# Optimization experiments

Hardware: AMD Instinct MI355X
Metric: run time of the kernel (lower is better)

Reference implementation:

```python
import jax, jax.numpy as jnp
import numpy as np

S = 4096          # seq_len (longformer-large-4096)
H = 1024          # hidden_size
FF = 3072         # ffnn_size (hardcoded)
G = 100           # number of gold mentions
MAX_SPAN = 30     # max_span_length
TOP_LAMBDA = 0.2
LN_EPS = 1e-5
MASK_VAL = 10000.0


def setup_inputs() -> dict:
    key = jax.random.key(0)
    ks = jax.random.split(key, 16)
    sc = 0.02
    sequence_output = jax.random.normal(ks[0], (1, S, H), jnp.float32)
    attention_mask = jnp.ones((1, S), jnp.int32)
    # valid gold spans: 1 <= start <= end < start + MAX_SPAN (so torch's >0 filter keeps all)
    gs = jax.random.randint(ks[1], (G,), 1, S - MAX_SPAN)
    gl = jax.random.randint(ks[2], (G,), 0, MAX_SPAN)
    gold_mentions = jnp.stack([gs, gs + gl], axis=1).astype(jnp.int32)  # [G, 2]
    inp = {
        'sequence_output': sequence_output,
        'attention_mask': attention_mask,
        'gold_mentions': gold_mentions,
        # start_mention_mlp
        'W_sm': jax.random.normal(ks[3], (H, FF), jnp.float32) * sc,
        'b_sm': jnp.zeros((FF,), jnp.float32),
        'g_sm': jnp.ones((FF,), jnp.float32),
        'beta_sm': jnp.zeros((FF,), jnp.float32),
        # end_mention_mlp
        'W_em': jax.random.normal(ks[4], (H, FF), jnp.float32) * sc,
        'b_em': jnp.zeros((FF,), jnp.float32),
        'g_em': jnp.ones((FF,), jnp.float32),
        'beta_em': jnp.zeros((FF,), jnp.float32),
        # classifiers
        'w_start': jax.random.normal(ks[5], (FF,), jnp.float32) * sc,
        'b_start': jnp.zeros((), jnp.float32),
        'w_end': jax.random.normal(ks[6], (FF,), jnp.float32) * sc,
        'b_end': jnp.zeros((), jnp.float32),
        'W_s2e': jax.random.normal(ks[7], (FF, FF), jnp.float32) * sc,
        'b_s2e': jnp.zeros((FF,), jnp.float32),
    }
    return inp


def _fcl(x, W, b, g, beta):
    # dense -> gelu (exact) -> layernorm (dropout is identity in eval)
    h = jax.nn.gelu(x @ W + b, approximate=False)
    mu = jnp.mean(h, axis=-1, keepdims=True)
    var = jnp.mean(jnp.square(h - mu), axis=-1, keepdims=True)
    return (h - mu) * jax.lax.rsqrt(var + LN_EPS) * g + beta


def _forward(sequence_output, attention_mask, gold_mentions,
             W_sm, b_sm, g_sm, beta_sm, W_em, b_em, g_em, beta_em,
             w_start, b_start, w_end, b_end, W_s2e, b_s2e):
    start_reps = _fcl(sequence_output, W_sm, b_sm, g_sm, beta_sm)  # [1,S,FF]
    end_reps = _fcl(sequence_output, W_em, b_em, g_em, beta_em)    # [1,S,FF]

    start_logits = jnp.einsum('bsf,f->bs', start_reps, w_start) + b_start  # [1,S]
    end_logits = jnp.einsum('bsf,f->bs', end_reps, w_end) + b_end          # [1,S]
    temp = start_reps @ W_s2e + b_s2e                                      # [1,S,FF]
    joint = jnp.einsum('bsf,btf->bst', temp, end_reps)                     # [1,S,S]
    mention_logits = joint + start_logits[:, :, None] + end_logits[:, None, :]

    # span mask: start <= end < start + MAX_SPAN (triu(0) then tril(MAX_SPAN-1))
    i = jnp.arange(S)
    mention_mask = ((i[:, None] <= i[None, :]) & (i[None, :] < i[:, None] + MAX_SPAN)
                    ).astype(jnp.float32)[None]  # [1,S,S]
    mention_logits = jnp.clip(mention_logits + (1.0 - mention_mask) * (-MASK_VAL),
                              -MASK_VAL, MASK_VAL)

    # top-k pruning; attention_mask is full so k is static: int(S * 0.2)
    max_k = int(S * TOP_LAMBDA)  # 819
    _, topk_1d = jax.lax.top_k(mention_logits.reshape(1, -1), max_k)  # [1,max_k]
    sorted_idx = jnp.sort(topk_1d, axis=-1)
    topk_start_ids = sorted_idx // S
    topk_end_ids = sorted_idx % S
    span_mask = jnp.ones((1, max_k), jnp.float32)

    # losses
    probs = jax.nn.sigmoid(mention_logits)  # [1,S,S]
    gstart = gold_mentions[:, 0]
    gend = gold_mentions[:, 1]
    gold_probs = probs[0, gstart, gend]
    # torch BCE clamps log at -100
    cost_gold = -jnp.mean(jnp.maximum(jnp.log(gold_probs), -100.0))
    junk = probs.at[0, gstart, gend].set(0.0)
    log1mp = jnp.maximum(jnp.log(1.0 - junk), -100.0)
    cost_junk = -jnp.sum(jnp.where(mention_mask == 1.0, log1mp, 0.0)) / jnp.sum(mention_mask)
    cost_is_mention = (cost_gold + cost_junk)[None]  # [1]

    return topk_start_ids, topk_end_ids, span_mask, sequence_output, cost_is_mention


def reference(sequence_output, attention_mask, gold_mentions,
              W_sm, b_sm, g_sm, beta_sm, W_em, b_em, g_em, beta_em,
              w_start, b_start, w_end, b_end, W_s2e, b_s2e):
    return _forward(sequence_output, attention_mask, gold_mentions,
                    W_sm, b_sm, g_sm, beta_sm, W_em, b_em, g_em, beta_em,
                    w_start, b_start, w_end, b_end, W_s2e, b_s2e)
```

## Files before the change

### kernel.cpp

```cpp
#include <hip/hip_runtime.h>
#include <math.h>

#define S 4096
#define H 1024
#define FF 3072
#define G 100
#define MAXSPAN 30
#define MAXK 819
#define NBAND (S * MAXSPAN)
#define BAND_COUNT 122445.0

#define O_START 0
#define O_END   819
#define O_MASK  1638
#define O_SEQ   2457
#define O_COST  (2457 + S * H)

typedef __bf16 bf16x8 __attribute__((ext_vector_type(8)));
typedef float f32x16 __attribute__((ext_vector_type(16)));


__device__ __forceinline__ float block_reduce_256(float x, volatile float* red) {
  #pragma unroll
  for (int off = 32; off > 0; off >>= 1) x += __shfl_down(x, off, 64);
  int wid = threadIdx.x >> 6;
  int lane = threadIdx.x & 63;
  __syncthreads();
  if (lane == 0) red[wid] = x;
  __syncthreads();
  return red[0] + red[1] + red[2] + red[3];
}

__device__ __forceinline__ float block_reduce_1024(float x, volatile float* red) {
  #pragma unroll
  for (int off = 32; off > 0; off >>= 1) x += __shfl_down(x, off, 64);
  int wid = threadIdx.x >> 6;
  int lane = threadIdx.x & 63;
  __syncthreads();
  if (lane == 0) red[wid] = x;
  __syncthreads();
  float s = 0.f;
  #pragma unroll
  for (int q = 0; q < 16; q++) s += red[q];
  return s;
}

__device__ __forceinline__ unsigned f2key(float f) {
  unsigned b = __float_as_uint(f);
  return (b & 0x80000000u) ? ~b : (b | 0x80000000u);
}

__device__ __forceinline__ unsigned short bf16_rne(float x) {
  unsigned u = __float_as_uint(x);
  unsigned r = ((u >> 16) & 1u) + 0x7FFFu;
  return (unsigned short)((u + r) >> 16);
}

__device__ __forceinline__ void split2(float x, unsigned short& h, unsigned short& l) {
  h = bf16_rne(x);
  float hf = __uint_as_float(((unsigned)h) << 16);
  l = bf16_rne(x - hf);
}

__device__ __forceinline__ void gld16(const void* g, void* l) {
  __builtin_amdgcn_global_load_lds(
      (const __attribute__((address_space(1))) unsigned int*)g,
      (__attribute__((address_space(3))) unsigned int*)l, 16, 0, 0);
}


__device__ __forceinline__ void pack_a_body(const float* __restrict__ A,
                                            float* __restrict__ Aout,
                                            unsigned short* __restrict__ hi,
                                            unsigned short* __restrict__ lo,
                                            int K, int bx, int by) {
  __shared__ float tile[32][33];
  const int t = threadIdx.x;
  const int tx = t & 31, ty8 = t >> 5;
  const int k0 = bx * 32, r0 = by * 32;
  #pragma unroll
  for (int r = ty8; r < 32; r += 8) {
    float v = A[(size_t)(r0 + r) * K + k0 + tx];
    tile[r][tx] = v;
    if (Aout) Aout[(size_t)(r0 + r) * K + k0 + tx] = v;
  }
  __syncthreads();
  if (t < 128) {
    const int kql = t >> 5;
    const int rl = t & 31;
    unsigned short h8[8], l8[8];
    #pragma unroll
    for (int s = 0; s < 8; s++) split2(tile[rl][kql * 8 + s], h8[s], l8[s]);
    const size_t panel = (size_t)(r0 >> 7);
    const int rloc = (r0 & 127) + rl;
    const size_t off = panel * (size_t)(128 * K) + (size_t)(k0 / 8 + kql) * 1024 + (size_t)rloc * 8;
    *(uint4*)(hi + off) = *(const uint4*)h8;
    *(uint4*)(lo + off) = *(const uint4*)l8;
  }
}

__device__ __forceinline__ void pack_ln_a_body(const float* __restrict__ A,
                                               const float* __restrict__ mu,
                                               const float* __restrict__ rstd,
                                               const float* __restrict__ g,
                                               const float* __restrict__ beta,
                                               unsigned short* __restrict__ hi,
                                               unsigned short* __restrict__ lo,
                                               int K, int bx, int by) {
  __shared__ float tile[32][33];
  const int t = threadIdx.x;
  const int tx = t & 31, ty8 = t >> 5;
  const int k0 = bx * 32, r0 = by * 32;
  #pragma unroll
  for (int r = ty8; r < 32; r += 8)
    tile[r][tx] = A[(size_t)(r0 + r) * K + k0 + tx];
  __syncthreads();
  if (t < 128) {
    const int kql = t >> 5;
    const int rl = t & 31;
    const int row = r0 + rl;
    const float m = mu[row], rs = rstd[row];
    float4 g0 = *(const float4*)(g + k0 + kql * 8);
    float4 g1 = *(const float4*)(g + k0 + kql * 8 + 4);
    float4 b0 = *(const float4*)(beta + k0 + kql * 8);
    float4 b1 = *(const float4*)(beta + k0 + kql * 8 + 4);
    float gv[8] = {g0.x, g0.y, g0.z, g0.w, g1.x, g1.y, g1.z, g1.w};
    float bv[8] = {b0.x, b0.y, b0.z, b0.w, b1.x, b1.y, b1.z, b1.w};
    unsigned short h8[8], l8[8];
    #pragma unroll
    for (int s = 0; s < 8; s++) {
      float v = (tile[rl][kql * 8 + s] - m) * rs * gv[s] + bv[s];
      split2(v, h8[s], l8[s]);
    }
    const size_t panel = (size_t)(r0 >> 7);
    const int rloc = (r0 & 127) + rl;
    const size_t off = panel * (size_t)(128 * K) + (size_t)(k0 / 8 + kql) * 1024 + (size_t)rloc * 8;
    *(uint4*)(hi + off) = *(const uint4*)h8;
    *(uint4*)(lo + off) = *(const uint4*)l8;
  }
}

__device__ __forceinline__ void pack_bt_body(const float* __restrict__ W,
                                             unsigned short* __restrict__ hi,
                                             unsigned short* __restrict__ lo,
                                             int K, int N, int bx, int by) {
  __shared__ float tile[32][33];
  const int t = threadIdx.x;
  const int tx = t & 31, ty8 = t >> 5;
  const int k0 = bx * 32, n0 = by * 32;
  #pragma unroll
  for (int r = ty8; r < 32; r += 8)
    tile[r][tx] = W[(size_t)(k0 + r) * N + n0 + tx];
  __syncthreads();
  if (t < 128) {
    const int kql = t >> 5;
    const int nl = t & 31;
    unsigned short h8[8], l8[8];
    #pragma unroll
    for (int s = 0; s < 8; s++) split2(tile[kql * 8 + s][nl], h8[s], l8[s]);
    const size_t panel = (size_t)(n0 >> 7);
    const int nloc = (n0 & 127) + nl;
    const size_t off = panel * (size_t)(128 * K) + (size_t)(k0 / 8 + kql) * 1024 + (size_t)nloc * 8;
    *(uint4*)(hi + off) = *(const uint4*)h8;
    *(uint4*)(lo + off) = *(const uint4*)l8;
  }
}

__global__ __launch_bounds__(256) void pack_head_kernel(const float* __restrict__ seq,
                                                        float* __restrict__ seq_out,
                                                        unsigned short* __restrict__ sh,
                                                        unsigned short* __restrict__ sl,
                                                        const float* __restrict__ W1,
                                                        const float* __restrict__ W2,
                                                        unsigned short* __restrict__ w1h,
                                                        unsigned short* __restrict__ w1l,
                                                        unsigned short* __restrict__ w2h,
                                                        unsigned short* __restrict__ w2l) {
  const int y = blockIdx.y;
  if (y < 128)      pack_a_body(seq, seq_out, sh, sl, H, blockIdx.x, y);
  else if (y < 224) pack_bt_body(W1, w1h, w1l, H, FF, blockIdx.x, y - 128);
  else              pack_bt_body(W2, w2h, w2l, H, FF, blockIdx.x, y - 224);
}

__global__ __launch_bounds__(256) void pack_mid_kernel(const float* __restrict__ bufS,
                                                       const float* __restrict__ muS,
                                                       const float* __restrict__ rstdS,
                                                       const float* __restrict__ g,
                                                       const float* __restrict__ beta,
                                                       unsigned short* __restrict__ ahi,
                                                       unsigned short* __restrict__ alo,
                                                       const float* __restrict__ Ws2e,
                                                       unsigned short* __restrict__ wbh,
                                                       unsigned short* __restrict__ wbl) {
  const int y = blockIdx.y;
  if (y < 128) pack_ln_a_body(bufS, muS, rstdS, g, beta, ahi, alo, FF, blockIdx.x, y);
  else         pack_bt_body(Ws2e, wbh, wbl, FF, FF, blockIdx.x, y - 128);
}


template <int EPI>
__device__ __forceinline__ void gemm_body(const char* cAh, const char* cAl,
                                          const char* cBh, const char* cBl,
                                          const float* __restrict__ bias,
                                          float* __restrict__ C,
                                          int bm, int bn, int N, int K,
                                          char* smem) {
  const int tid = threadIdx.x;
  const int lane = tid & 63;
  const int wid = __builtin_amdgcn_readfirstlane(tid >> 6);
  const int wm = wid >> 1, wn = wid & 1;
  const int lb = lane * 16;
  const int ldsq = wid * 2048;

  const int khalf = lane >> 5;
  const int r31 = lane & 31;
  const int abase = khalf * 2048 + (wm * 64 + r31) * 16;
  const int bbase = khalf * 2048 + (wn * 64 + r31) * 16;

  f32x16 acc[2][2];
  #pragma unroll
  for (int a = 0; a < 2; a++)
    #pragma unroll
    for (int b = 0; b < 2; b++)
      #pragma unroll
      for (int r = 0; r < 16; r++) acc[a][b][r] = 0.0f;

  auto stage = [&](int buf, int k0) {
    const size_t qb = (size_t)((k0 >> 3) + wid) * 2048 + lb;
    char* sbuf = smem + buf * 32768 + ldsq;
    gld16(cAh + qb,        sbuf +     0);
    gld16(cAh + qb + 1024, sbuf +     0 + 1024);
    gld16(cAl + qb,        sbuf +  8192);
    gld16(cAl + qb + 1024, sbuf +  8192 + 1024);
    gld16(cBh + qb,        sbuf + 16384);
    gld16(cBh + qb + 1024, sbuf + 16384 + 1024);
    gld16(cBl + qb,        sbuf + 24576);
    gld16(cBl + qb + 1024, sbuf + 24576 + 1024);
  };

  stage(0, 0);
  for (int k0 = 0; k0 < K; k0 += 32) {
    const int cur = (k0 >> 5) & 1;
    __syncthreads();
    if (k0 + 32 < K) stage(cur ^ 1, k0 + 32);
    const char* sm = smem + cur * 32768;

    bf16x8 ah[2][2], al[2][2], bh[2][2], bl[2][2];
    #pragma unroll
    for (int ks = 0; ks < 2; ks++) {
      #pragma unroll
      for (int mt = 0; mt < 2; mt++) {
        ah[ks][mt] = *(const bf16x8*)(sm +     0 + ks * 4096 + abase + mt * 512);
        al[ks][mt] = *(const bf16x8*)(sm +  8192 + ks * 4096 + abase + mt * 512);
      }
      #pragma unroll
      for (int nt = 0; nt < 2; nt++) {
        bh[ks][nt] = *(const bf16x8*)(sm + 16384 + ks * 4096 + bbase + nt * 512);
        bl[ks][nt] = *(const bf16x8*)(sm + 24576 + ks * 4096 + bbase + nt * 512);
      }
    }
    #pragma unroll
    for (int ks = 0; ks < 2; ks++)
      #pragma unroll
      for (int mt = 0; mt < 2; mt++)
        #pragma unroll
        for (int nt = 0; nt < 2; nt++) {
          acc[mt][nt] = __builtin_amdgcn_mfma_f32_32x32x16_bf16(ah[ks][mt], bh[ks][nt], acc[mt][nt], 0, 0, 0);
          acc[mt][nt] = __builtin_amdgcn_mfma_f32_32x32x16_bf16(al[ks][mt], bh[ks][nt], acc[mt][nt], 0, 0, 0);
          acc[mt][nt] = __builtin_amdgcn_mfma_f32_32x32x16_bf16(ah[ks][mt], bl[ks][nt], acc[mt][nt], 0, 0, 0);
        }
  }

  #pragma unroll
  for (int mt = 0; mt < 2; mt++) {
    #pragma unroll
    for (int nt = 0; nt < 2; nt++) {
      const int colg = bn + wn * 64 + nt * 32 + r31;
      const float bb = bias[colg];
      #pragma unroll
      for (int reg = 0; reg < 16; reg++) {
        const int rowl = (reg & 3) + 8 * (reg >> 2) + 4 * khalf;
        const int rowg = bm + wm * 64 + mt * 32 + rowl;
        float v = acc[mt][nt][reg] + bb;
        if (EPI == 1) v = 0.5f * v * (1.0f + erff(v * 0.70710678118654752f));
        C[(size_t)rowg * N + colg] = v;
      }
    }
  }
}

__global__ __launch_bounds__(256) void gemm_mfma_kernel(const unsigned short* __restrict__ Ahi,
                                                        const unsigned short* __restrict__ Alo,
                                                        const unsigned short* __restrict__ Bhi,
                                                        const unsigned short* __restrict__ Blo,
                                                        const float* __restrict__ bias,
                                                        float* __restrict__ C,
                                                        int N, int K) {
  __shared__ __align__(16) char smem[65536];
  const size_t panAb = (size_t)blockIdx.y * (size_t)(128 * K) * 2;
  const size_t panBb = (size_t)blockIdx.x * (size_t)(128 * K) * 2;
  gemm_body<0>((const char*)Ahi + panAb, (const char*)Alo + panAb,
               (const char*)Bhi + panBb, (const char*)Blo + panBb,
               bias, C, blockIdx.y * 128, blockIdx.x * 128, N, K, smem);
}

__global__ __launch_bounds__(256) void gemm_mfma_dual_kernel(const unsigned short* __restrict__ Ahi,
                                                             const unsigned short* __restrict__ Alo,
                                                             const unsigned short* __restrict__ B1hi,
                                                             const unsigned short* __restrict__ B1lo,
                                                             const unsigned short* __restrict__ B2hi,
                                                             const unsigned short* __restrict__ B2lo,
                                                             const float* __restrict__ bias1,
                                                             const float* __restrict__ bias2,
                                                             float* __restrict__ C1,
                                                             float* __restrict__ C2,
                                                             int N, int K) {
  __shared__ __align__(16) char smem[65536];
  const int zb = blockIdx.z;
  const unsigned short* Bhi = zb ? B2hi : B1hi;
  const unsigned short* Blo = zb ? B2lo : B1lo;
  const float* bias = zb ? bias2 : bias1;
  float* C = zb ? C2 : C1;
  const size_t panAb = (size_t)blockIdx.y * (size_t)(128 * K) * 2;
  const size_t panBb = (size_t)blockIdx.x * (size_t)(128 * K) * 2;
  gemm_body<1>((const char*)Ahi + panAb, (const char*)Alo + panAb,
               (const char*)Bhi + panBb, (const char*)Blo + panBb,
               bias, C, blockIdx.y * 128, blockIdx.x * 128, N, K, smem);
}


__global__ __launch_bounds__(256) void ln_stats_kernel(const float* __restrict__ HbS,
                                                       const float* __restrict__ HbE,
                                                       const float* __restrict__ gS,
                                                       const float* __restrict__ betaS,
                                                       const float* __restrict__ wS,
                                                       const float* __restrict__ bS,
                                                       const float* __restrict__ gE,
                                                       const float* __restrict__ betaE,
                                                       const float* __restrict__ wE,
                                                       const float* __restrict__ bE,
                                                       float* __restrict__ slog,
                                                       float* __restrict__ elog,
                                                       float* __restrict__ muS,
                                                       float* __restrict__ rstdS,
                                                       float* __restrict__ muE,
                                                       float* __restrict__ rstdE) {
  __shared__ float red[4];
  const int row = blockIdx.x, tid = threadIdx.x;
  const int br = blockIdx.y;
  const float* Hb = br ? HbE : HbS;
  const float* g = br ? gE : gS;
  const float* beta = br ? betaE : betaS;
  const float* w = br ? wE : wS;
  const float* bsc = br ? bE : bS;
  const float* h = Hb + (size_t)row * FF;

  float4 v[3];
  float s = 0.0f;
  #pragma unroll
  for (int t = 0; t < 3; t++) {
    v[t] = *(const float4*)(h + tid * 4 + t * 1024);
    s += v[t].x + v[t].y + v[t].z + v[t].w;
  }
  float mu = block_reduce_256(s, red) * (1.0f / (float)FF);

  float s2 = 0.0f;
  #pragma unroll
  for (int t = 0; t < 3; t++) {
    float dx = v[t].x - mu, dy = v[t].y - mu, dz = v[t].z - mu, dw = v[t].w - mu;
    s2 += dx * dx + dy * dy + dz * dz + dw * dw;
  }
  float var = block_reduce_256(s2, red) * (1.0f / (float)FF);
  float rstd = rsqrtf(var + 1e-5f);

  float dot = 0.0f;
  #pragma unroll
  for (int t = 0; t < 3; t++) {
    int idx = tid * 4 + t * 1024;
    float4 gv = *(const float4*)(g + idx);
    float4 bv = *(const float4*)(beta + idx);
    float4 wv = *(const float4*)(w + idx);
    float rx = (v[t].x - mu) * rstd * gv.x + bv.x;
    float ry = (v[t].y - mu) * rstd * gv.y + bv.y;
    float rz = (v[t].z - mu) * rstd * gv.z + bv.z;
    float rw = (v[t].w - mu) * rstd * gv.w + bv.w;
    dot += rx * wv.x + ry * wv.y + rz * wv.z + rw * wv.w;
  }
  float dt = block_reduce_256(dot, red);
  if (tid == 0) {
    if (br) { elog[row] = dt + bsc[0]; muE[row] = mu; rstdE[row] = rstd; }
    else    { slog[row] = dt + bsc[0]; muS[row] = mu; rstdS[row] = rstd; }
  }
}


__global__ __launch_bounds__(256) void band_joint_kernel(const float* __restrict__ T,
                                                         const float* __restrict__ Eraw,
                                                         const float* __restrict__ muE,
                                                         const float* __restrict__ rstdE,
                                                         const float* __restrict__ gE,
                                                         const float* __restrict__ betaE,
                                                         const float* __restrict__ sl,
                                                         const float* __restrict__ el,
                                                         float* __restrict__ band,
                                                         double* __restrict__ jacc,
                                                         unsigned* __restrict__ hist16) {
  __shared__ float Elds[45][260];
  __shared__ float red[4];
  const int t = threadIdx.x;
  const int bx = blockIdx.x;
  const int sbx = (bx & 7) * 32 + (bx >> 3);
  const int i0 = sbx * 16;
  const int r_l = t >> 4, c = t & 15;

  float accd[MAXSPAN];
  #pragma unroll
  for (int d = 0; d < MAXSPAN; d++) accd[d] = 0.0f;

  for (int k0 = 0; k0 < FF; k0 += 256) {
    const float* trow = T + (size_t)(i0 + r_l) * FF + k0 + c * 16;
    float4 tv0 = *(const float4*)(trow + 0);
    float4 tv1 = *(const float4*)(trow + 4);
    float4 tv2 = *(const float4*)(trow + 8);
    float4 tv3 = *(const float4*)(trow + 12);
    __syncthreads();
    for (int rr = t >> 6; rr < 45; rr += 4) {
      int gr = i0 + rr;
      int cc = (t & 63) * 4;
      float4 rv = {0.f, 0.f, 0.f, 0.f};
      if (gr < S) {
        float4 ev = *(const float4*)(Eraw + (size_t)gr * FF + k0 + cc);
        float m = muE[gr], rs = rstdE[gr];
        float4 gv = *(const float4*)(gE + k0 + cc);
        float4 bv = *(const float4*)(betaE + k0 + cc);
        rv.x = (ev.x - m) * rs * gv.x + bv.x;
        rv.y = (ev.y - m) * rs * gv.y + bv.y;
        rv.z = (ev.z - m) * rs * gv.z + bv.z;
        rv.w = (ev.w - m) * rs * gv.w + bv.w;
      }
      *(float4*)&Elds[rr][cc] = rv;
    }
    __syncthreads();
    #pragma unroll
    for (int d = 0; d < MAXSPAN; d++) {
      const float* er = &Elds[r_l + d][c * 16];
      float4 e0 = *(const float4*)(er + 0);
      float4 e1 = *(const float4*)(er + 4);
      float4 e2 = *(const float4*)(er + 8);
      float4 e3 = *(const float4*)(er + 12);
      accd[d] += tv0.x * e0.x + tv0.y * e0.y + tv0.z * e0.z + tv0.w * e0.w
               + tv1.x * e1.x + tv1.y * e1.y + tv1.z * e1.z + tv1.w * e1.w
               + tv2.x * e2.x + tv2.y * e2.y + tv2.z * e2.z + tv2.w * e2.w
               + tv3.x * e3.x + tv3.y * e3.y + tv3.z * e3.z + tv3.w * e3.w;
    }
  }

  const int i = i0 + r_l;
  const float my_sl = sl[i];
  float jsum = 0.0f;
  #pragma unroll
  for (int d = 0; d < MAXSPAN; d++) {
    float v = accd[d];
    v += __shfl_down(v, 8, 16);
    v += __shfl_down(v, 4, 16);
    v += __shfl_down(v, 2, 16);
    v += __shfl_down(v, 1, 16);
    if (c == 0) {
      int j = i + d;
      if (j < S) {
        float vv = v + my_sl + el[j];
        vv = fminf(fmaxf(vv, -10000.0f), 10000.0f);
        band[i * MAXSPAN + d] = vv;
        atomicAdd(&hist16[f2key(vv) >> 16], 1u);
        float p = 1.0f / (1.0f + expf(-vv));
        jsum += fmaxf(logf(1.0f - p), -100.0f);
      } else {
        band[i * MAXSPAN + d] = -1e30f;
      }
    }
  }
  float tot = block_reduce_256(jsum, red);
  if (t == 0) atomicAdd(jacc, (double)tot);
}


__global__ __launch_bounds__(1024) void topk_finalize_kernel(const float* __restrict__ band,
                                                             const int* __restrict__ gold,
                                                             const double* __restrict__ jacc,
                                                             const unsigned* __restrict__ hist16,
                                                             float* __restrict__ out) {
  __shared__ int csum[1024];
  __shared__ unsigned sh_T16;
  __shared__ int sh_remk;
  __shared__ int sh_chunk, sh_above;
  __shared__ int idxbuf[1024];
  __shared__ unsigned tkey[256];
  __shared__ int tidx[256];
  __shared__ int cnt_gt, cnt_eq;
  __shared__ int sb[1024];
  __shared__ int gcell[G];
  __shared__ float redf[16];
  const int tid = threadIdx.x;

  int s = 0;
  #pragma unroll 8
  for (int q = 0; q < 64; q++) s += (int)hist16[tid * 64 + q];
  csum[tid] = s;
  __syncthreads();
  for (int off = 1; off < 1024; off <<= 1) {
    int v = (tid + off < 1024) ? csum[tid + off] : 0;
    __syncthreads();
    csum[tid] += v;
    __syncthreads();
  }
  {
    int nxt = (tid < 1023) ? csum[tid + 1] : 0;
    if (csum[tid] >= MAXK && nxt < MAXK) { sh_chunk = tid; sh_above = nxt; }
  }
  __syncthreads();
  if (tid == 0) {
    int cum = sh_above;
    int b = sh_chunk * 64 + 63;
    for (;; b--) {
      int h = (int)hist16[b];
      if (cum + h >= MAXK || b == sh_chunk * 64) { sh_T16 = (unsigned)b; sh_remk = MAXK - cum; break; }
      cum += h;
    }
  }
  __syncthreads();
  const unsigned T16 = sh_T16;
  int remk = sh_remk;

  if (tid == 0) { cnt_gt = 0; cnt_eq = 0; }
  __syncthreads();
  for (int e = tid; e < NBAND; e += 1024) {
    unsigned key = f2key(band[e]);
    unsigned k16 = key >> 16;
    if (k16 >= T16) {
      int i = e / MAXSPAN, d = e - i * MAXSPAN;
      int fi = i * S + i + d;
      if (k16 > T16) {
        int p = atomicAdd(&cnt_gt, 1);
        if (p < 1024) idxbuf[p] = fi;
      } else {
        int p = atomicAdd(&cnt_eq, 1);
        if (p < 256) { tkey[p] = key; tidx[p] = fi; }
      }
    }
  }
  __syncthreads();
  if (tid == 0) {
    int ngt = cnt_gt < 1024 ? cnt_gt : 1024;
    int ne = cnt_eq < 256 ? cnt_eq : 256;
    for (int a2 = 1; a2 < ne; a2++) {
      unsigned kv = tkey[a2]; int iv = tidx[a2];
      int b2 = a2 - 1;
      while (b2 >= 0 && (tkey[b2] < kv || (tkey[b2] == kv && tidx[b2] > iv))) {
        tkey[b2 + 1] = tkey[b2]; tidx[b2 + 1] = tidx[b2]; b2--;
      }
      tkey[b2 + 1] = kv; tidx[b2 + 1] = iv;
    }
    int take = remk < ne ? remk : ne;
    for (int q = 0; q < take; q++)
      if (ngt + q < 1024) idxbuf[ngt + q] = tidx[q];
  }
  __syncthreads();

  sb[tid] = (tid < MAXK) ? idxbuf[tid] : 0x7FFFFFFF;
  __syncthreads();
  for (int ksz = 2; ksz <= 1024; ksz <<= 1) {
    for (int jj = ksz >> 1; jj > 0; jj >>= 1) {
      int ixj = tid ^ jj;
      if (ixj > tid) {
        int a2 = sb[tid], b2 = sb[ixj];
        bool up = ((tid & ksz) == 0);
        if (up ? (a2 > b2) : (a2 < b2)) { sb[tid] = b2; sb[ixj] = a2; }
      }
      __syncthreads();
    }
  }
  if (tid < MAXK) {
    int fi = sb[tid];
    out[O_START + tid] = (float)(fi >> 12);
    out[O_END + tid]   = (float)(fi & 4095);
    out[O_MASK + tid]  = 1.0f;
  }

  if (tid < G) {
    int gs = gold[2 * tid], ge = gold[2 * tid + 1];
    gcell[tid] = gs * MAXSPAN + (ge - gs);
  }
  __syncthreads();
  float tg = 0.0f, tj = 0.0f;
  if (tid < G) {
    int cell = gcell[tid];
    float x = band[cell];
    float p = 1.0f / (1.0f + expf(-x));
    tg = fmaxf(logf(p), -100.0f);
    bool first = true;
    for (int q = 0; q < tid; q++)
      if (gcell[q] == cell) { first = false; break; }
    if (first) tj = fmaxf(logf(1.0f - p), -100.0f);
  }
  float sg = block_reduce_1024(tg, redf);
  float sj = block_reduce_1024(tj, redf);
  if (tid == 0) {
    double junk = *jacc - (double)sj;
    double cost = -((double)sg / (double)G) - (junk / BAND_COUNT);
    out[O_COST] = (float)cost;
  }
}


extern "C" void kernel_launch(void* const* d_in, const int* in_sizes, int n_in,
                              void* d_out, int out_size, void* d_ws, size_t ws_size,
                              hipStream_t stream) {
  (void)in_sizes; (void)n_in; (void)out_size; (void)ws_size;
  const float* seq    = (const float*)d_in[0];
  const int*   gold   = (const int*)d_in[2];
  const float* W_sm   = (const float*)d_in[3];
  const float* b_sm   = (const float*)d_in[4];
  const float* g_sm   = (const float*)d_in[5];
  const float* be_sm  = (const float*)d_in[6];
  const float* W_em   = (const float*)d_in[7];
  const float* b_em   = (const float*)d_in[8];
  const float* g_em   = (const float*)d_in[9];
  const float* be_em  = (const float*)d_in[10];
  const float* w_st   = (const float*)d_in[11];
  const float* b_st   = (const float*)d_in[12];
  const float* w_en   = (const float*)d_in[13];
  const float* b_en   = (const float*)d_in[14];
  const float* W_s2e  = (const float*)d_in[15];
  const float* b_s2e  = (const float*)d_in[16];
  float* out = (float*)d_out;
  char* ws = (char*)d_ws;

  const size_t SZ_REP = (size_t)S * FF * 4;
  float*  bufS = (float*)(ws);
  float*  bufE = (float*)(ws + SZ_REP);
  float*  bufT = (float*)(ws + 2 * SZ_REP);
  char* R3 = ws + 3 * SZ_REP;
  unsigned short* seqhi = (unsigned short*)R3;
  unsigned short* seqlo = (unsigned short*)(R3 + (size_t)S * H * 2);
  unsigned short* a3hi  = (unsigned short*)R3;
  unsigned short* a3lo  = (unsigned short*)(R3 + (size_t)S * FF * 2);
  char* R4 = ws + 4 * SZ_REP;
  const size_t SZ_W12 = (size_t)H * FF * 2;
  unsigned short* wb1hi = (unsigned short*)R4;
  unsigned short* wb1lo = (unsigned short*)(R4 + SZ_W12);
  unsigned short* wb2hi = (unsigned short*)(R4 + 2 * SZ_W12);
  unsigned short* wb2lo = (unsigned short*)(R4 + 3 * SZ_W12);
  unsigned short* wbhi = (unsigned short*)R4;
  unsigned short* wblo = (unsigned short*)(R4 + (size_t)FF * FF * 2);
  char* R5 = R4 + 2 * (size_t)FF * FF * 2;
  float*    band   = (float*)R5;
  unsigned* hist16 = (unsigned*)(R5 + (size_t)NBAND * 4);
  double*   jacc   = (double*)(R5 + (size_t)NBAND * 4 + 262144);
  float*    slog   = (float*)(R5 + (size_t)NBAND * 4 + 262144 + 64);
  float*  elog  = slog + S;
  float*  muS   = elog + S;
  float*  rstdS = muS + S;
  float*  muE   = rstdS + S;
  float*  rstdE = muE + S;

  hipMemsetAsync(hist16, 0, 262144 + 64 + 8, stream);

  dim3 gg(FF / 128, S / 128);
  dim3 gg2(FF / 128, S / 128, 2);

  pack_head_kernel<<<dim3(32, 320), 256, 0, stream>>>(seq, out + O_SEQ, seqhi, seqlo,
                                                      W_sm, W_em, wb1hi, wb1lo, wb2hi, wb2lo);
  gemm_mfma_dual_kernel<<<gg2, 256, 0, stream>>>(seqhi, seqlo, wb1hi, wb1lo, wb2hi, wb2lo,
                                                 b_sm, b_em, bufS, bufE, FF, H);
  ln_stats_kernel<<<dim3(S, 2), 256, 0, stream>>>(bufS, bufE, g_sm, be_sm, w_st, b_st,
                                                  g_em, be_em, w_en, b_en,
                                                  slog, elog, muS, rstdS, muE, rstdE);
  pack_mid_kernel<<<dim3(96, 224), 256, 0, stream>>>(bufS, muS, rstdS, g_sm, be_sm,
                                                     a3hi, a3lo, W_s2e, wbhi, wblo);
  gemm_mfma_kernel<<<gg, 256, 0, stream>>>(a3hi, a3lo, wbhi, wblo, b_s2e, bufT, FF, FF);

  band_joint_kernel<<<S / 16, 256, 0, stream>>>(bufT, bufE, muE, rstdE, g_em, be_em,
                                                slog, elog, band, jacc, hist16);

  topk_finalize_kernel<<<1, 1024, 0, stream>>>(band, gold, jacc, hist16, out);
}
```

Measured before the change: 811.9 us.

## Enlarge GEMM tiles to 256x192 with 8 waves, 4-slot pipeline and grid swizzle

Replaces the 128x128, 4-wave double-buffered split-bf16 GEMM with a 256x192 tile computed by 8 waves, each holding a 2x3 set of MFMA accumulators. Global-to-LDS loads now go through a 4-slot ring with three stages in flight, explicit vmcnt waits and raw barriers, and MFMA issue runs at raised priority. A grid swizzle groups blocks so neighbouring blocks share A and B panels in cache. The aim is more operand reuse per loaded byte and better overlap of loads with MFMA work. The cost is heavier register pressure and a grid of only 256 or 512 blocks, which may not fill the CUs evenly.

```diff
diff --git a/kernel.cpp b/kernel.cpp
--- a/kernel.cpp
+++ b/kernel.cpp
@@ -197,85 +197,112 @@
   else         pack_bt_body(Ws2e, wbh, wbl, FF, FF, blockIdx.x, y - 128);
 }
 
+#define SLOTB 28672
+#define A_STR 8192
+#define B_BASE 16384
+#define B_STR 6144
 
 template <int EPI>
-__device__ __forceinline__ void gemm_body(const char* cAh, const char* cAl,
-                                          const char* cBh, const char* cBl,
-                                          const float* __restrict__ bias,
-                                          float* __restrict__ C,
-                                          int bm, int bn, int N, int K,
-                                          char* smem) {
+__device__ __forceinline__ void gemm8_body(const char* __restrict__ cAh, const char* __restrict__ cAl,
+                                           const char* __restrict__ cBh, const char* __restrict__ cBl,
+                                           const float* __restrict__ bias,
+                                           float* __restrict__ C,
+                                           int bm, int bn, int N, int K,
+                                           char* smem) {
   const int tid = threadIdx.x;
   const int lane = tid & 63;
   const int wid = __builtin_amdgcn_readfirstlane(tid >> 6);
   const int wm = wid >> 1, wn = wid & 1;
-  const int lb = lane * 16;
-  const int ldsq = wid * 2048;
-
   const int khalf = lane >> 5;
   const int r31 = lane & 31;
-  const int abase = khalf * 2048 + (wm * 64 + r31) * 16;
-  const int bbase = khalf * 2048 + (wn * 64 + r31) * 16;
-
-  f32x16 acc[2][2];
-  #pragma unroll
-  for (int a = 0; a < 2; a++)
-    #pragma unroll
-    for (int b = 0; b < 2; b++)
+  const size_t PS = (size_t)256 * (size_t)K;
+
+  const char* lsrc[4];
+  int ldst[4];
+  #pragma unroll
+  for (int i = 0; i < 4; i++) { lsrc[i] = cAh; ldst[i] = 0; }
+  if (wid < 7) {
+    #pragma unroll
+    for (int i = 0; i < 4; i++) {
+      int q = wid * 4 + i;
+      if (q < 16) {
+        int str = q >> 3, r = q & 7, kql = r >> 2, u = r & 3;
+        lsrc[i] = (str ? cAl : cAh) + (size_t)((bm >> 7) + (u >> 1)) * PS
+                + (size_t)(kql * 2048 + (u & 1) * 1024 + lane * 16);
+        ldst[i] = str * A_STR + kql * 4096 + u * 1024;
+      } else {
+        int qq = q - 16;
+        int str = qq / 6, r = qq % 6, kql = r / 3, v = r % 3;
+        int gcol = bn + 64 * v;
+        lsrc[i] = (str ? cBl : cBh) + (size_t)(gcol >> 7) * PS
+                + (size_t)(kql * 2048 + ((gcol >> 6) & 1) * 1024 + lane * 16);
+        ldst[i] = B_BASE + str * B_STR + kql * 3072 + v * 1024;
+      }
+    }
+  }
+
+  const int aoff = khalf * 4096 + (wm * 64 + r31) * 16;
+  const int boff = B_BASE + khalf * 3072 + (wn * 96 + r31) * 16;
+
+  f32x16 acc[2][3];
+  #pragma unroll
+  for (int mt = 0; mt < 2; mt++)
+    #pragma unroll
+    for (int nt = 0; nt < 3; nt++)
       #pragma unroll
-      for (int r = 0; r < 16; r++) acc[a][b][r] = 0.0f;
-
-  auto stage = [&](int buf, int k0) {
-    const size_t qb = (size_t)((k0 >> 3) + wid) * 2048 + lb;
-    char* sbuf = smem + buf * 32768 + ldsq;
-    gld16(cAh + qb,        sbuf +     0);
-    gld16(cAh + qb + 1024, sbuf +     0 + 1024);
-    gld16(cAl + qb,        sbuf +  8192);
-    gld16(cAl + qb + 1024, sbuf +  8192 + 1024);
-    gld16(cBh + qb,        sbuf + 16384);
-    gld16(cBh + qb + 1024, sbuf + 16384 + 1024);
-    gld16(cBl + qb,        sbuf + 24576);
-    gld16(cBl + qb + 1024, sbuf + 24576 + 1024);
+      for (int r = 0; r < 16; r++) acc[mt][nt][r] = 0.0f;
+
+  auto stage = [&](int h) {
+    if (wid < 7) {
+      char* sb = smem + (h & 3) * SLOTB;
+      const size_t ko = (size_t)h * 4096;
+      #pragma unroll
+      for (int i = 0; i < 4; i++) gld16(lsrc[i] + ko, sb + ldst[i]);
+    }
   };
 
-  stage(0, 0);
-  for (int k0 = 0; k0 < K; k0 += 32) {
-    const int cur = (k0 >> 5) & 1;
-    __syncthreads();
-    if (k0 + 32 < K) stage(cur ^ 1, k0 + 32);
-    const char* sm = smem + cur * 32768;
-
-    bf16x8 ah[2][2], al[2][2], bh[2][2], bl[2][2];
-    #pragma unroll
-    for (int ks = 0; ks < 2; ks++) {
+  const int NH = K >> 4;
+
+  stage(0); stage(1); stage(2);
+  asm volatile("s_waitcnt vmcnt(8)" ::: "memory");
+  __builtin_amdgcn_s_barrier();
+
+  for (int p = 0; p < NH; ++p) {
+    const char* sm = smem + (p & 3) * SLOTB;
+    bf16x8 ah[2], al[2], bh[3], bl[3];
+    #pragma unroll
+    for (int mt = 0; mt < 2; mt++) {
+      ah[mt] = *(const bf16x8*)(sm + aoff + mt * 512);
+      al[mt] = *(const bf16x8*)(sm + A_STR + aoff + mt * 512);
+    }
+    #pragma unroll
+    for (int nt = 0; nt < 3; nt++) {
+      bh[nt] = *(const bf16x8*)(sm + boff + nt * 512);
+      bl[nt] = *(const bf16x8*)(sm + B_STR + boff + nt * 512);
+    }
+    if (p + 3 < NH) stage(p + 3);
+    asm volatile("s_waitcnt lgkmcnt(0)" ::: "memory");
+    __builtin_amdgcn_s_setprio(1);
+    #pragma unroll
+    for (int mt = 0; mt < 2; mt++)
       #pragma unroll
-      for (int mt = 0; mt < 2; mt++) {
-        ah[ks][mt] = *(const bf16x8*)(sm +     0 + ks * 4096 + abase + mt * 512);
-        al[ks][mt] = *(const bf16x8*)(sm +  8192 + ks * 4096 + abase + mt * 512);
+      for (int nt = 0; nt < 3; nt++) {
+        acc[mt][nt] = __builtin_amdgcn_mfma_f32_32x32x16_bf16(ah[mt], bh[nt], acc[mt][nt], 0, 0, 0);
+        acc[mt][nt] = __builtin_amdgcn_mfma_f32_32x32x16_bf16(al[mt], bh[nt], acc[mt][nt], 0, 0, 0);
+        acc[mt][nt] = __builtin_amdgcn_mfma_f32_32x32x16_bf16(ah[mt], bl[nt], acc[mt][nt], 0, 0, 0);
       }
-      #pragma unroll
-      for (int nt = 0; nt < 2; nt++) {
-        bh[ks][nt] = *(const bf16x8*)(sm + 16384 + ks * 4096 + bbase + nt * 512);
-        bl[ks][nt] = *(const bf16x8*)(sm + 24576 + ks * 4096 + bbase + nt * 512);
-      }
-    }
-    #pragma unroll
-    for (int ks = 0; ks < 2; ks++)
-      #pragma unroll
-      for (int mt = 0; mt < 2; mt++)
-        #pragma unroll
-        for (int nt = 0; nt < 2; nt++) {
-          acc[mt][nt] = __builtin_amdgcn_mfma_f32_32x32x16_bf16(ah[ks][mt], bh[ks][nt], acc[mt][nt], 0, 0, 0);
-          acc[mt][nt] = __builtin_amdgcn_mfma_f32_32x32x16_bf16(al[ks][mt], bh[ks][nt], acc[mt][nt], 0, 0, 0);
-          acc[mt][nt] = __builtin_amdgcn_mfma_f32_32x32x16_bf16(ah[ks][mt], bl[ks][nt], acc[mt][nt], 0, 0, 0);
-        }
+    __builtin_amdgcn_s_setprio(0);
+    if (p + 4 < NH)       { asm volatile("s_waitcnt vmcnt(8)" ::: "memory"); }
+    else if (p + 3 == NH) { asm volatile("s_waitcnt vmcnt(4)" ::: "memory"); }
+    else if (p + 2 == NH) { asm volatile("s_waitcnt vmcnt(0)" ::: "memory"); }
+    if (p + 1 < NH) __builtin_amdgcn_s_barrier();
   }
 
   #pragma unroll
   for (int mt = 0; mt < 2; mt++) {
     #pragma unroll
-    for (int nt = 0; nt < 2; nt++) {
-      const int colg = bn + wn * 64 + nt * 32 + r31;
+    for (int nt = 0; nt < 3; nt++) {
+      const int colg = bn + wn * 96 + nt * 32 + r31;
       const float bb = bias[colg];
       #pragma unroll
       for (int reg = 0; reg < 16; reg++) {
@@ -289,22 +316,29 @@
   }
 }
 
-__global__ __launch_bounds__(256) void gemm_mfma_kernel(const unsigned short* __restrict__ Ahi,
+__device__ __forceinline__ void grid_swizzle_16x16(int& bx, int& by) {
+  const int lin = blockIdx.y * 16 + blockIdx.x;
+  const int X = lin & 7, c = lin >> 3;
+  bx = (X & 3) * 4 + (c & 3);
+  by = (X >> 2) * 8 + (c >> 2);
+}
+
+__global__ __launch_bounds__(512) void gemm_mfma_kernel(const unsigned short* __restrict__ Ahi,
                                                         const unsigned short* __restrict__ Alo,
                                                         const unsigned short* __restrict__ Bhi,
                                                         const unsigned short* __restrict__ Blo,
                                                         const float* __restrict__ bias,
                                                         float* __restrict__ C,
                                                         int N, int K) {
-  __shared__ __align__(16) char smem[65536];
-  const size_t panAb = (size_t)blockIdx.y * (size_t)(128 * K) * 2;
-  const size_t panBb = (size_t)blockIdx.x * (size_t)(128 * K) * 2;
-  gemm_body<0>((const char*)Ahi + panAb, (const char*)Alo + panAb,
-               (const char*)Bhi + panBb, (const char*)Blo + panBb,
-               bias, C, blockIdx.y * 128, blockIdx.x * 128, N, K, smem);
-}
-
-__global__ __launch_bounds__(256) void gemm_mfma_dual_kernel(const unsigned short* __restrict__ Ahi,
+  __shared__ __align__(16) char smem[4 * SLOTB];
+  int bx, by;
+  grid_swizzle_16x16(bx, by);
+  gemm8_body<0>((const char*)Ahi, (const char*)Alo,
+                (const char*)Bhi, (const char*)Blo,
+                bias, C, by * 256, bx * 192, N, K, smem);
+}
+
+__global__ __launch_bounds__(512) void gemm_mfma_dual_kernel(const unsigned short* __restrict__ Ahi,
                                                              const unsigned short* __restrict__ Alo,
                                                              const unsigned short* __restrict__ B1hi,
                                                              const unsigned short* __restrict__ B1lo,
@@ -315,17 +349,17 @@
                                                              float* __restrict__ C1,
                                                              float* __restrict__ C2,
                                                              int N, int K) {
-  __shared__ __align__(16) char smem[65536];
+  __shared__ __align__(16) char smem[4 * SLOTB];
   const int zb = blockIdx.z;
   const unsigned short* Bhi = zb ? B2hi : B1hi;
   const unsigned short* Blo = zb ? B2lo : B1lo;
   const float* bias = zb ? bias2 : bias1;
   float* C = zb ? C2 : C1;
-  const size_t panAb = (size_t)blockIdx.y * (size_t)(128 * K) * 2;
-  const size_t panBb = (size_t)blockIdx.x * (size_t)(128 * K) * 2;
-  gemm_body<1>((const char*)Ahi + panAb, (const char*)Alo + panAb,
-               (const char*)Bhi + panBb, (const char*)Blo + panBb,
-               bias, C, blockIdx.y * 128, blockIdx.x * 128, N, K, smem);
+  int bx, by;
+  grid_swizzle_16x16(bx, by);
+  gemm8_body<1>((const char*)Ahi, (const char*)Alo,
+                (const char*)Bhi, (const char*)Blo,
+                bias, C, by * 256, bx * 192, N, K, smem);
 }
 
 
@@ -665,19 +699,19 @@
 
   hipMemsetAsync(hist16, 0, 262144 + 64 + 8, stream);
 
-  dim3 gg(FF / 128, S / 128);
-  dim3 gg2(FF / 128, S / 128, 2);
+  dim3 gg(16, 16);
+  dim3 gg2(16, 16, 2);
 
   pack_head_kernel<<<dim3(32, 320), 256, 0, stream>>>(seq, out + O_SEQ, seqhi, seqlo,
                                                       W_sm, W_em, wb1hi, wb1lo, wb2hi, wb2lo);
-  gemm_mfma_dual_kernel<<<gg2, 256, 0, stream>>>(seqhi, seqlo, wb1hi, wb1lo, wb2hi, wb2lo,
+  gemm_mfma_dual_kernel<<<gg2, 512, 0, stream>>>(seqhi, seqlo, wb1hi, wb1lo, wb2hi, wb2lo,
                                                  b_sm, b_em, bufS, bufE, FF, H);
   ln_stats_kernel<<<dim3(S, 2), 256, 0, stream>>>(bufS, bufE, g_sm, be_sm, w_st, b_st,
                                                   g_em, be_em, w_en, b_en,
                                                   slog, elog, muS, rstdS, muE, rstdE);
   pack_mid_kernel<<<dim3(96, 224), 256, 0, stream>>>(bufS, muS, rstdS, g_sm, be_sm,
                                                      a3hi, a3lo, W_s2e, wbhi, wblo);
-  gemm_mfma_kernel<<<gg, 256, 0, stream>>>(a3hi, a3lo, wbhi, wblo, b_s2e, bufT, FF, FF);
+  gemm_mfma_kernel<<<gg, 512, 0, stream>>>(a3hi, a3lo, wbhi, wblo, b_s2e, bufT, FF, FF);
 
   band_joint_kernel<<<S / 16, 256, 0, stream>>>(bufT, bufE, muE, rstdE, g_em, be_em,
                                                 slog, elog, band, jacc, hist16);
```

Result: faster. 785.5 us (-3.2%).
